# Kernel tuning notes

Hardware: AMD Instinct MI355X
Metric: run time of the kernel (lower is better)

The kernel has to match this reference:

```python
import jax, jax.numpy as jnp
import numpy as np

N_HEADS = 16
HEAD_SZ = 64

def setup_inputs() -> dict:
    key = jax.random.key(0)
    ks = jax.random.split(key, 6)
    E = 1024
    s = 1.0 / np.sqrt(E)
    return {
        "x": jax.random.normal(ks[0], (2, 2048, E), dtype=jnp.float32),
        "Wq": jax.random.normal(ks[1], (E, N_HEADS * HEAD_SZ), dtype=jnp.float32) * s,
        "Wk": jax.random.normal(ks[2], (E, N_HEADS * HEAD_SZ), dtype=jnp.float32) * s,
        "Wv": jax.random.normal(ks[3], (E, N_HEADS * HEAD_SZ), dtype=jnp.float32) * s,
        "Wp": jax.random.normal(ks[4], (N_HEADS * HEAD_SZ, E), dtype=jnp.float32) * s,
        "bp": jnp.zeros((E,), dtype=jnp.float32),
    }

def reference(x, Wq, Wk, Wv, Wp, bp):
    # flavor="masked": causal self-attention, pdrop=0 -> dropout is identity
    B, S, E = x.shape
    H, D = N_HEADS, HEAD_SZ
    q = (x @ Wq).reshape(B, S, H, D).transpose(0, 2, 1, 3)  # [B,H,S,D]
    k = (x @ Wk).reshape(B, S, H, D).transpose(0, 2, 1, 3)
    v = (x @ Wv).reshape(B, S, H, D).transpose(0, 2, 1, 3)
    scores = jnp.einsum("bhqd,bhkd->bhqk", q, k) / jnp.sqrt(jnp.float32(D))
    causal = jnp.tril(jnp.ones((S, S), dtype=bool))  # [S,S]
    scores = jnp.where(causal, scores, -jnp.inf)
    attn = jax.nn.softmax(scores, axis=-1)
    out = jnp.einsum("bhqk,bhkd->bhqd", attn, v)  # [B,H,S,D]
    out = out.transpose(0, 2, 1, 3).reshape(B, S, H * D)
    return out @ Wp + bp
```

## Files before the change

### kernel.cpp

```cpp
#include <hip/hip_runtime.h>
#include <hip/hip_bf16.h>
#include <math.h>

using bf16 = __hip_bfloat16;
typedef __attribute__((ext_vector_type(8))) short short8;
typedef __attribute__((ext_vector_type(4))) float floatx4;

#define MFMA16(a, b, c) __builtin_amdgcn_mfma_f32_16x16x32_bf16((a), (b), (c), 0, 0, 0)

__device__ __forceinline__ void gll16(const void* g, void* l) {
  __builtin_amdgcn_global_load_lds((__attribute__((address_space(1))) void*)(uintptr_t)g,
                                   (__attribute__((address_space(3))) void*)l, 16, 0, 0);
}

__global__ void detect_bias_k(const unsigned short* __restrict__ x,
                              const void* __restrict__ bsrc,
                              bf16* __restrict__ bdst, int* __restrict__ flag) {
  __shared__ int cnt;
  if (threadIdx.x == 0) cnt = 0;
  __syncthreads();
  int local = 0;
  for (int i = threadIdx.x; i < 8192; i += 256) {
    unsigned short v = x[2 * i];
    if (((v >> 7) & 0xFF) == 0xFF) local++;
  }
  if (local) atomicAdd(&cnt, local);
  __syncthreads();
  int f = (cnt > 0) ? 1 : 0;
  if (threadIdx.x == 0) *flag = f;
  for (int i = threadIdx.x; i < 1024; i += 256)
    bdst[i] = f ? __float2bfloat16(((const float*)bsrc)[i]) : ((const bf16*)bsrc)[i];
}

__global__ __launch_bounds__(256) void prep_k(const void* __restrict__ xin,
                                              bf16* __restrict__ xb,
                                              const void* __restrict__ W0,
                                              const void* __restrict__ W1,
                                              const void* __restrict__ W2,
                                              const void* __restrict__ W3,
                                              bf16* __restrict__ Wt,
                                              bf16* __restrict__ Wpt,
                                              const int* __restrict__ flag) {
  bool f32 = (*flag != 0);
  int z = blockIdx.z;
  if (z < 2) {
    int tid = threadIdx.y * 32 + threadIdx.x;
    int blockLin = z * 1024 + blockIdx.y * 32 + blockIdx.x;
    int idx = blockLin * 2048 + tid * 8;
    if (f32) {
      const float4* p = reinterpret_cast<const float4*>((const float*)xin + idx);
      float4 a = p[0], b = p[1];
      union { bf16 h[8]; uint4 u; } U;
      U.h[0] = __float2bfloat16(a.x); U.h[1] = __float2bfloat16(a.y);
      U.h[2] = __float2bfloat16(a.z); U.h[3] = __float2bfloat16(a.w);
      U.h[4] = __float2bfloat16(b.x); U.h[5] = __float2bfloat16(b.y);
      U.h[6] = __float2bfloat16(b.z); U.h[7] = __float2bfloat16(b.w);
      *reinterpret_cast<uint4*>(xb + idx) = U.u;
    } else {
      *reinterpret_cast<uint4*>(xb + idx) =
          *reinterpret_cast<const uint4*>((const bf16*)xin + idx);
    }
    return;
  }
  const void* src = (z == 2) ? W0 : (z == 3) ? W1 : (z == 4) ? W2 : W3;
  bf16* dst = (z == 5) ? Wpt : (Wt + (size_t)(z - 2) * 1024 * 1024);
  __shared__ float tsh[32][33];
  int tx = threadIdx.x, ty = threadIdx.y;
  int k0 = blockIdx.y * 32, n0 = blockIdx.x * 32;
  for (int i = 0; i < 4; i++) {
    size_t off = (size_t)(k0 + ty + i * 8) * 1024 + n0 + tx;
    tsh[ty + i * 8][tx] = f32 ? ((const float*)src)[off]
                              : __bfloat162float(((const bf16*)src)[off]);
  }
  __syncthreads();
  for (int i = 0; i < 4; i++)
    dst[(size_t)(n0 + ty + i * 8) * 1024 + k0 + tx] = __float2bfloat16(tsh[tx][ty + i * 8]);
}

__global__ __launch_bounds__(512) void vtrans_k(const bf16* __restrict__ QKV,
                                                bf16* __restrict__ VT) {
  __shared__ bf16 t[64][66];
  int tx = threadIdx.x, ty = threadIdx.y;
  int s0 = blockIdx.x * 64, bh = blockIdx.y;
  int b = bh >> 4, h = bh & 15;
  size_t rowb = (size_t)b * 2048;
  int hv = 2048 + h * 64;
#pragma unroll
  for (int i = 0; i < 8; i++)
    t[i * 8 + ty][tx] = QKV[(rowb + s0 + i * 8 + ty) * 3072 + hv + tx];
  __syncthreads();
#pragma unroll
  for (int i = 0; i < 8; i++)
    VT[((size_t)bh * 64 + i * 8 + ty) * 2048 + s0 + tx] = t[tx][i * 8 + ty];
}

__global__ __launch_bounds__(256) void gemm_bt128(const bf16* __restrict__ A, int lda,
                                                  const bf16* __restrict__ Bt, int ldb,
                                                  void* __restrict__ C, int ldc,
                                                  const bf16* __restrict__ bias, int K,
                                                  const int* __restrict__ outflag) {
  __shared__ bf16 As[2][128 * 32];
  __shared__ bf16 Bs[2][128 * 32];
  int t = threadIdx.x;
  int w = t >> 6, lane = t & 63;
  int g = lane >> 4, c = lane & 15;
  int wm = (w >> 1) * 64, wn = (w & 1) * 64;

  int lin = blockIdx.x + 24 * blockIdx.y;
  int xcd = lin & 7;
  int sl = lin >> 3;
  int mt = (xcd >> 1) * 8 + (sl & 7);
  int nt = (xcd & 1) * 12 + (sl >> 3);
  int m0 = mt * 128, n0 = nt * 128;

  int sr = w * 32 + (lane >> 2);
  int sc = (lane & 3) * 8;
  const bf16* Ab = A + (size_t)(m0 + sr) * lda + sc;
  const bf16* Bb = Bt + (size_t)(n0 + sr) * ldb + sc;
  int lofs = (w * 32) * 32;

  floatx4 acc[4][4] = {};

  for (int k0 = 0; k0 < K; k0 += 64) {
    __syncthreads();
#pragma unroll
    for (int h = 0; h < 2; h++) {
      gll16(Ab + k0 + h * 32, &As[h][lofs]);
      gll16(Ab + k0 + h * 32 + (size_t)16 * lda, &As[h][lofs + 16 * 32]);
      gll16(Bb + k0 + h * 32, &Bs[h][lofs]);
      gll16(Bb + k0 + h * 32 + (size_t)16 * ldb, &Bs[h][lofs + 16 * 32]);
    }
    __syncthreads();
#pragma unroll
    for (int h = 0; h < 2; h++) {
      short8 af[4], bf[4];
#pragma unroll
      for (int i = 0; i < 4; i++) {
        af[i] = *reinterpret_cast<const short8*>(&As[h][(wm + i * 16 + c) * 32 + g * 8]);
        bf[i] = *reinterpret_cast<const short8*>(&Bs[h][(wn + i * 16 + c) * 32 + g * 8]);
      }
#pragma unroll
      for (int i = 0; i < 4; i++)
#pragma unroll
        for (int j = 0; j < 4; j++) acc[i][j] = MFMA16(af[i], bf[j], acc[i][j]);
    }
  }

  bool f32out = (outflag != nullptr) && (*outflag != 0);
#pragma unroll
  for (int i = 0; i < 4; i++) {
    int rbase = m0 + wm + i * 16 + g * 4;
#pragma unroll
    for (int j = 0; j < 4; j++) {
      int col = n0 + wn + j * 16 + c;
      float bv = bias ? __bfloat162float(bias[col]) : 0.f;
#pragma unroll
      for (int r = 0; r < 4; r++) {
        size_t off = (size_t)(rbase + r) * ldc + col;
        float v = acc[i][j][r] + bv;
        if (f32out) ((float*)C)[off] = v;
        else ((bf16*)C)[off] = __float2bfloat16(v);
      }
    }
  }
}

__global__ __launch_bounds__(256) void gemm_bt64(const bf16* __restrict__ A, int lda,
                                                 const bf16* __restrict__ Bt, int ldb,
                                                 void* __restrict__ C, int ldc,
                                                 const bf16* __restrict__ bias, int K,
                                                 const int* __restrict__ outflag) {
  __shared__ bf16 As[2][128 * 32];
  __shared__ bf16 Bs[2][64 * 32];
  int t = threadIdx.x;
  int w = t >> 6, lane = t & 63;
  int g = lane >> 4, c = lane & 15;
  int wm = (w >> 1) * 64, wn = (w & 1) * 32;

  int lin = blockIdx.x + 16 * blockIdx.y;
  int xcd = lin & 7;
  int sl = lin >> 3;
  int mt = (xcd >> 1) * 8 + (sl & 7);
  int nt = (xcd & 1) * 8 + (sl >> 3);
  int m0 = mt * 128, n0 = nt * 64;

  int sr = (lane >> 2);
  int sc = (lane & 3) * 8;
  const bf16* Ab = A + (size_t)(m0 + w * 32 + sr) * lda + sc;
  const bf16* Bb = Bt + (size_t)(n0 + w * 16 + sr) * ldb + sc;
  int laofs = (w * 32) * 32;
  int lbofs = (w * 16) * 32;

  floatx4 acc[4][2] = {};

  for (int k0 = 0; k0 < K; k0 += 64) {
    __syncthreads();
#pragma unroll
    for (int h = 0; h < 2; h++) {
      gll16(Ab + k0 + h * 32, &As[h][laofs]);
      gll16(Ab + k0 + h * 32 + (size_t)16 * lda, &As[h][laofs + 16 * 32]);
      gll16(Bb + k0 + h * 32, &Bs[h][lbofs]);
    }
    __syncthreads();
#pragma unroll
    for (int h = 0; h < 2; h++) {
      short8 af[4], bf[2];
#pragma unroll
      for (int i = 0; i < 4; i++)
        af[i] = *reinterpret_cast<const short8*>(&As[h][(wm + i * 16 + c) * 32 + g * 8]);
#pragma unroll
      for (int j = 0; j < 2; j++)
        bf[j] = *reinterpret_cast<const short8*>(&Bs[h][(wn + j * 16 + c) * 32 + g * 8]);
#pragma unroll
      for (int i = 0; i < 4; i++)
#pragma unroll
        for (int j = 0; j < 2; j++) acc[i][j] = MFMA16(af[i], bf[j], acc[i][j]);
    }
  }

  bool f32out = (outflag != nullptr) && (*outflag != 0);
#pragma unroll
  for (int i = 0; i < 4; i++) {
    int rbase = m0 + wm + i * 16 + g * 4;
#pragma unroll
    for (int j = 0; j < 2; j++) {
      int col = n0 + wn + j * 16 + c;
      float bv = bias ? __bfloat162float(bias[col]) : 0.f;
#pragma unroll
      for (int r = 0; r < 4; r++) {
        size_t off = (size_t)(rbase + r) * ldc + col;
        float v = acc[i][j][r] + bv;
        if (f32out) ((float*)C)[off] = v;
        else ((bf16*)C)[off] = __float2bfloat16(v);
      }
    }
  }
}

__global__ __launch_bounds__(512, 4) void attn_lds2(bf16* __restrict__ QKV,
                                                    const bf16* __restrict__ VT) {
  const int S = 2048, LD = 3072;
  __shared__ bf16 Ks[2][2][64 * 32];
  __shared__ bf16 Vs[2][2][64 * 32];
  __shared__ bf16 Pb[8][16 * 72];

  int t = threadIdx.x, w = t >> 6, lane = t & 63, g = lane >> 4, c = lane & 15;

  int r = blockIdx.x + 16 * blockIdx.y;
  int xcd = r & 7;
  int s = r >> 3;
  int m = s >> 4;
  int u = s & 15;
  int bh = xcd + 8 * m;
  int qt = (m & 2) ? (15 - u) : u;

  int b = bh >> 4, h = bh & 15;
  int qbase = qt * 128;
  size_t rowb = (size_t)b * S;
  int hq = h * 64, hk = 1024 + h * 64;
  const bf16* Vt = VT + (size_t)bh * 64 * 2048;
  bf16* pb = Pb[w];

  int su = (w & 3) * 16 + (lane >> 2);
  int sc = (lane & 3) * 8;
  const bf16* Kg = &QKV[(rowb + su) * LD + hk + sc];
  const bf16* Vg = &Vt[(size_t)su * 2048 + sc];
  int sofs = ((w & 3) * 16) * 32;

  short8 qf[2];
#pragma unroll
  for (int hf = 0; hf < 2; hf++)
    qf[hf] = *reinterpret_cast<const short8*>(
        &QKV[(rowb + qbase + w * 16 + c) * LD + hq + hf * 32 + g * 8]);

  floatx4 o[4] = {};
  float lsum = 0.f;
  int qrow = qbase + w * 16 + c;

  int nkt = 2 * qt + 2;
  if (w < 4) {
    gll16(Kg, &Ks[0][0][sofs]);
    gll16(Kg + 32, &Ks[0][1][sofs]);
  } else {
    gll16(Vg, &Vs[0][0][sofs]);
    gll16(Vg + 32, &Vs[0][1][sofs]);
  }

  for (int kt = 0; kt < nkt; kt++) {
    int kbase = kt * 64;
    int cur = kt & 1;
    __syncthreads();
    if (kt + 1 < nkt) {
      int nb = cur ^ 1;
      size_t kofs = (size_t)(kbase + 64);
      if (w < 4) {
        gll16(Kg + kofs * LD, &Ks[nb][0][sofs]);
        gll16(Kg + kofs * LD + 32, &Ks[nb][1][sofs]);
      } else {
        gll16(Vg + kofs, &Vs[nb][0][sofs]);
        gll16(Vg + kofs + 32, &Vs[nb][1][sofs]);
      }
    }

    short8 kf[4][2];
#pragma unroll
    for (int nt = 0; nt < 4; nt++)
#pragma unroll
      for (int hf = 0; hf < 2; hf++)
        kf[nt][hf] =
            *reinterpret_cast<const short8*>(&Ks[cur][hf][(nt * 16 + c) * 32 + g * 8]);

    floatx4 sv[4];
    __builtin_amdgcn_s_setprio(1);
#pragma unroll
    for (int nt = 0; nt < 4; nt++) {
      floatx4 z = {};
      z = MFMA16(kf[nt][0], qf[0], z);
      z = MFMA16(kf[nt][1], qf[1], z);
      sv[nt] = z;
    }
    __builtin_amdgcn_s_setprio(0);

    bool diag = (kbase + 63 > qbase + w * 16);
#pragma unroll
    for (int nt = 0; nt < 4; nt++) {
      int kcol0 = kbase + nt * 16 + g * 4;
#pragma unroll
      for (int rr = 0; rr < 4; rr++) {
        float arg = fmaf(sv[nt][rr], 0.18033688f, -23.083120f);
        if (diag && (kcol0 + rr > qrow)) arg = -1e30f;
        float p = exp2f(arg);
        lsum += p;
        sv[nt][rr] = p;
      }
    }

#pragma unroll
    for (int nt = 0; nt < 4; nt++) {
      union { bf16 h4[4]; uint2 u2; } U;
      U.h4[0] = __float2bfloat16(sv[nt][0]);
      U.h4[1] = __float2bfloat16(sv[nt][1]);
      U.h4[2] = __float2bfloat16(sv[nt][2]);
      U.h4[3] = __float2bfloat16(sv[nt][3]);
      *reinterpret_cast<uint2*>(&pb[c * 72 + nt * 16 + g * 4]) = U.u2;
    }
    asm volatile("s_waitcnt lgkmcnt(0)" ::: "memory");
    short8 pf0 = *reinterpret_cast<const short8*>(&pb[c * 72 + g * 8]);
    short8 pf1 = *reinterpret_cast<const short8*>(&pb[c * 72 + 32 + g * 8]);

    __builtin_amdgcn_s_setprio(1);
#pragma unroll
    for (int dt = 0; dt < 4; dt++) {
      short8 vf0 = *reinterpret_cast<const short8*>(&Vs[cur][0][(dt * 16 + c) * 32 + g * 8]);
      short8 vf1 = *reinterpret_cast<const short8*>(&Vs[cur][1][(dt * 16 + c) * 32 + g * 8]);
      o[dt] = MFMA16(pf0, vf0, o[dt]);
      o[dt] = MFMA16(pf1, vf1, o[dt]);
    }
    __builtin_amdgcn_s_setprio(0);
  }

  lsum += __shfl_xor(lsum, 16);
  lsum += __shfl_xor(lsum, 32);
  float lrec = 1.0f / lsum;
  float l_r[4];
#pragma unroll
  for (int rr = 0; rr < 4; rr++) l_r[rr] = __shfl(lrec, g * 4 + rr);

#pragma unroll
  for (int dt = 0; dt < 4; dt++)
#pragma unroll
    for (int rr = 0; rr < 4; rr++) {
      float v = o[dt][rr] * l_r[rr];
      QKV[(rowb + qbase + w * 16 + g * 4 + rr) * LD + hq + dt * 16 + c] =
          __float2bfloat16(v);
    }
}

extern "C" void kernel_launch(void* const* d_in, const int* in_sizes, int n_in,
                              void* d_out, int out_size, void* d_ws, size_t ws_size,
                              hipStream_t stream) {
  char* ws = (char*)d_ws;
  const size_t MB = 1024 * 1024;
  int* flag = (int*)ws;
  bf16* bias = (bf16*)(ws + 4096);
  bf16* xb = (bf16*)(ws + 1 * MB);
  bf16* Wt = (bf16*)(ws + 9 * MB);
  bf16* Wpt = (bf16*)(ws + 15 * MB);
  bf16* QKV = (bf16*)(ws + 17 * MB);
  bf16* VT = xb;

  detect_bias_k<<<1, 256, 0, stream>>>((const unsigned short*)d_in[0], d_in[5], bias, flag);
  prep_k<<<dim3(32, 32, 6), dim3(32, 8), 0, stream>>>(d_in[0], xb, d_in[1], d_in[2],
                                                      d_in[3], d_in[4], Wt, Wpt, flag);

  gemm_bt128<<<dim3(24, 32), 256, 0, stream>>>(xb, 1024, Wt, 1024, QKV, 3072, nullptr,
                                               1024, nullptr);
  vtrans_k<<<dim3(32, 32), dim3(64, 8), 0, stream>>>(QKV, VT);
  attn_lds2<<<dim3(16, 32), 512, 0, stream>>>(QKV, VT);
  gemm_bt64<<<dim3(16, 32), 256, 0, stream>>>(QKV, 3072, Wpt, 1024, d_out, 1024, bias,
                                              1024, flag);
}
```

Baseline: 202.8 us.

## Fuse V transpose into projection GEMM epilogue and vectorize GEMM stores

```diff
diff --git a/kernel.cpp b/kernel.cpp
--- a/kernel.cpp
+++ b/kernel.cpp
@@ -77,28 +77,9 @@
     dst[(size_t)(n0 + ty + i * 8) * 1024 + k0 + tx] = __float2bfloat16(tsh[tx][ty + i * 8]);
 }
 
-__global__ __launch_bounds__(512) void vtrans_k(const bf16* __restrict__ QKV,
-                                                bf16* __restrict__ VT) {
-  __shared__ bf16 t[64][66];
-  int tx = threadIdx.x, ty = threadIdx.y;
-  int s0 = blockIdx.x * 64, bh = blockIdx.y;
-  int b = bh >> 4, h = bh & 15;
-  size_t rowb = (size_t)b * 2048;
-  int hv = 2048 + h * 64;
-#pragma unroll
-  for (int i = 0; i < 8; i++)
-    t[i * 8 + ty][tx] = QKV[(rowb + s0 + i * 8 + ty) * 3072 + hv + tx];
-  __syncthreads();
-#pragma unroll
-  for (int i = 0; i < 8; i++)
-    VT[((size_t)bh * 64 + i * 8 + ty) * 2048 + s0 + tx] = t[tx][i * 8 + ty];
-}
-
-__global__ __launch_bounds__(256) void gemm_bt128(const bf16* __restrict__ A, int lda,
-                                                  const bf16* __restrict__ Bt, int ldb,
-                                                  void* __restrict__ C, int ldc,
-                                                  const bf16* __restrict__ bias, int K,
-                                                  const int* __restrict__ outflag) {
+__global__ __launch_bounds__(256) void gemm_qk(const bf16* __restrict__ A, int lda,
+                                               const bf16* __restrict__ Bt, int ldb,
+                                               bf16* __restrict__ C, int ldc, int K) {
   __shared__ bf16 As[2][128 * 32];
   __shared__ bf16 Bs[2][128 * 32];
   int t = threadIdx.x;
@@ -106,11 +87,10 @@
   int g = lane >> 4, c = lane & 15;
   int wm = (w >> 1) * 64, wn = (w & 1) * 64;
 
-  int lin = blockIdx.x + 24 * blockIdx.y;
-  int xcd = lin & 7;
-  int sl = lin >> 3;
+  int lin = blockIdx.x + 16 * blockIdx.y;
+  int xcd = lin & 7, sl = lin >> 3;
   int mt = (xcd >> 1) * 8 + (sl & 7);
-  int nt = (xcd & 1) * 12 + (sl >> 3);
+  int nt = (xcd & 1) * 8 + (sl >> 3);
   int m0 = mt * 128, n0 = nt * 128;
 
   int sr = w * 32 + (lane >> 2);
@@ -142,25 +122,84 @@
 #pragma unroll
       for (int i = 0; i < 4; i++)
 #pragma unroll
+        for (int j = 0; j < 4; j++) acc[i][j] = MFMA16(bf[j], af[i], acc[i][j]);
+    }
+  }
+
+#pragma unroll
+  for (int i = 0; i < 4; i++) {
+    int row = m0 + wm + i * 16 + c;
+#pragma unroll
+    for (int j = 0; j < 4; j++) {
+      int colb = n0 + wn + j * 16 + g * 4;
+      union { bf16 h4[4]; uint2 u2; } U;
+#pragma unroll
+      for (int r = 0; r < 4; r++) U.h4[r] = __float2bfloat16(acc[i][j][r]);
+      *reinterpret_cast<uint2*>(&C[(size_t)row * ldc + colb]) = U.u2;
+    }
+  }
+}
+
+__global__ __launch_bounds__(256) void gemm_v(const bf16* __restrict__ A, int lda,
+                                              const bf16* __restrict__ Bt, int ldb,
+                                              bf16* __restrict__ VT, int K) {
+  __shared__ bf16 As[2][128 * 32];
+  __shared__ bf16 Bs[2][128 * 32];
+  int t = threadIdx.x;
+  int w = t >> 6, lane = t & 63;
+  int g = lane >> 4, c = lane & 15;
+  int wm = (w >> 1) * 64, wn = (w & 1) * 64;
+
+  int lin = blockIdx.x + 8 * blockIdx.y;
+  int xcd = lin & 7, sl = lin >> 3;
+  int m0 = sl * 128, n0 = xcd * 128;
+
+  int sr = w * 32 + (lane >> 2);
+  int sc = (lane & 3) * 8;
+  const bf16* Ab = A + (size_t)(m0 + sr) * lda + sc;
+  const bf16* Bb = Bt + (size_t)(n0 + sr) * ldb + sc;
+  int lofs = (w * 32) * 32;
+
+  floatx4 acc[4][4] = {};
+
+  for (int k0 = 0; k0 < K; k0 += 64) {
+    __syncthreads();
+#pragma unroll
+    for (int h = 0; h < 2; h++) {
+      gll16(Ab + k0 + h * 32, &As[h][lofs]);
+      gll16(Ab + k0 + h * 32 + (size_t)16 * lda, &As[h][lofs + 16 * 32]);
+      gll16(Bb + k0 + h * 32, &Bs[h][lofs]);
+      gll16(Bb + k0 + h * 32 + (size_t)16 * ldb, &Bs[h][lofs + 16 * 32]);
+    }
+    __syncthreads();
+#pragma unroll
+    for (int h = 0; h < 2; h++) {
+      short8 af[4], bf[4];
+#pragma unroll
+      for (int i = 0; i < 4; i++) {
+        af[i] = *reinterpret_cast<const short8*>(&As[h][(wm + i * 16 + c) * 32 + g * 8]);
+        bf[i] = *reinterpret_cast<const short8*>(&Bs[h][(wn + i * 16 + c) * 32 + g * 8]);
+      }
+#pragma unroll
+      for (int i = 0; i < 4; i++)
+#pragma unroll
         for (int j = 0; j < 4; j++) acc[i][j] = MFMA16(af[i], bf[j], acc[i][j]);
     }
   }
 
-  bool f32out = (outflag != nullptr) && (*outflag != 0);
+  int b = m0 >> 11;
+  int sbase = (m0 & 2047);
 #pragma unroll
   for (int i = 0; i < 4; i++) {
-    int rbase = m0 + wm + i * 16 + g * 4;
+    int s0v = sbase + wm + i * 16 + g * 4;
 #pragma unroll
     for (int j = 0; j < 4; j++) {
-      int col = n0 + wn + j * 16 + c;
-      float bv = bias ? __bfloat162float(bias[col]) : 0.f;
-#pragma unroll
-      for (int r = 0; r < 4; r++) {
-        size_t off = (size_t)(rbase + r) * ldc + col;
-        float v = acc[i][j][r] + bv;
-        if (f32out) ((float*)C)[off] = v;
-        else ((bf16*)C)[off] = __float2bfloat16(v);
-      }
+      int colv = n0 + wn + j * 16 + c;
+      int h = colv >> 6, d = colv & 63;
+      union { bf16 h4[4]; uint2 u2; } U;
+#pragma unroll
+      for (int r = 0; r < 4; r++) U.h4[r] = __float2bfloat16(acc[i][j][r]);
+      *reinterpret_cast<uint2*>(&VT[((size_t)(b * 16 + h) * 64 + d) * 2048 + s0v]) = U.u2;
     }
   }
 }
@@ -178,8 +217,7 @@
   int wm = (w >> 1) * 64, wn = (w & 1) * 32;
 
   int lin = blockIdx.x + 16 * blockIdx.y;
-  int xcd = lin & 7;
-  int sl = lin >> 3;
+  int xcd = lin & 7, sl = lin >> 3;
   int mt = (xcd >> 1) * 8 + (sl & 7);
   int nt = (xcd & 1) * 8 + (sl >> 3);
   int m0 = mt * 128, n0 = nt * 64;
@@ -214,24 +252,34 @@
 #pragma unroll
       for (int i = 0; i < 4; i++)
 #pragma unroll
-        for (int j = 0; j < 2; j++) acc[i][j] = MFMA16(af[i], bf[j], acc[i][j]);
+        for (int j = 0; j < 2; j++) acc[i][j] = MFMA16(bf[j], af[i], acc[i][j]);
     }
   }
 
   bool f32out = (outflag != nullptr) && (*outflag != 0);
 #pragma unroll
   for (int i = 0; i < 4; i++) {
-    int rbase = m0 + wm + i * 16 + g * 4;
+    int row = m0 + wm + i * 16 + c;
 #pragma unroll
     for (int j = 0; j < 2; j++) {
-      int col = n0 + wn + j * 16 + c;
-      float bv = bias ? __bfloat162float(bias[col]) : 0.f;
-#pragma unroll
-      for (int r = 0; r < 4; r++) {
-        size_t off = (size_t)(rbase + r) * ldc + col;
-        float v = acc[i][j][r] + bv;
-        if (f32out) ((float*)C)[off] = v;
-        else ((bf16*)C)[off] = __float2bfloat16(v);
+      int colb = n0 + wn + j * 16 + g * 4;
+      float bv[4] = {0.f, 0.f, 0.f, 0.f};
+      if (bias) {
+        union { bf16 h4[4]; uint2 u2; } B;
+        B.u2 = *reinterpret_cast<const uint2*>(&bias[colb]);
+#pragma unroll
+        for (int r = 0; r < 4; r++) bv[r] = __bfloat162float(B.h4[r]);
+      }
+      if (f32out) {
+        float4 V;
+        V.x = acc[i][j][0] + bv[0]; V.y = acc[i][j][1] + bv[1];
+        V.z = acc[i][j][2] + bv[2]; V.w = acc[i][j][3] + bv[3];
+        *reinterpret_cast<float4*>(&((float*)C)[(size_t)row * ldc + colb]) = V;
+      } else {
+        union { bf16 h4[4]; uint2 u2; } U;
+#pragma unroll
+        for (int r = 0; r < 4; r++) U.h4[r] = __float2bfloat16(acc[i][j][r] + bv[r]);
+        *reinterpret_cast<uint2*>(&((bf16*)C)[(size_t)row * ldc + colb]) = U.u2;
       }
     }
   }
@@ -239,7 +287,7 @@
 
 __global__ __launch_bounds__(512, 4) void attn_lds2(bf16* __restrict__ QKV,
                                                     const bf16* __restrict__ VT) {
-  const int S = 2048, LD = 3072;
+  const int S = 2048, LD = 2048;
   __shared__ bf16 Ks[2][2][64 * 32];
   __shared__ bf16 Vs[2][2][64 * 32];
   __shared__ bf16 Pb[8][16 * 72];
@@ -386,17 +434,17 @@
   bf16* xb = (bf16*)(ws + 1 * MB);
   bf16* Wt = (bf16*)(ws + 9 * MB);
   bf16* Wpt = (bf16*)(ws + 15 * MB);
-  bf16* QKV = (bf16*)(ws + 17 * MB);
-  bf16* VT = xb;
+  bf16* QK = (bf16*)(ws + 17 * MB);
+  bf16* VT = (bf16*)(ws + 33 * MB);
 
   detect_bias_k<<<1, 256, 0, stream>>>((const unsigned short*)d_in[0], d_in[5], bias, flag);
   prep_k<<<dim3(32, 32, 6), dim3(32, 8), 0, stream>>>(d_in[0], xb, d_in[1], d_in[2],
                                                       d_in[3], d_in[4], Wt, Wpt, flag);
 
-  gemm_bt128<<<dim3(24, 32), 256, 0, stream>>>(xb, 1024, Wt, 1024, QKV, 3072, nullptr,
-                                               1024, nullptr);
-  vtrans_k<<<dim3(32, 32), dim3(64, 8), 0, stream>>>(QKV, VT);
-  attn_lds2<<<dim3(16, 32), 512, 0, stream>>>(QKV, VT);
-  gemm_bt64<<<dim3(16, 32), 256, 0, stream>>>(QKV, 3072, Wpt, 1024, d_out, 1024, bias,
+  gemm_qk<<<dim3(16, 32), 256, 0, stream>>>(xb, 1024, Wt, 1024, QK, 2048, 1024);
+  gemm_v<<<dim3(8, 32), 256, 0, stream>>>(xb, 1024, Wt + (size_t)2048 * 1024, 1024, VT,
+                                          1024);
+  attn_lds2<<<dim3(16, 32), 512, 0, stream>>>(QK, VT);
+  gemm_bt64<<<dim3(16, 32), 256, 0, stream>>>(QK, 2048, Wpt, 1024, d_out, 1024, bias,
                                               1024, flag);
 }
```

New measurement: 212.3 us. +4.7%, slower.
